# Performance work log

Hardware: AMD Instinct MI355X
Metric: run time of the kernel (lower is better)

## Reference

```python
import jax, jax.numpy as jnp
import numpy as np

B, T, C = 4, 2048, 1024
N_HEADS = 16
HEAD_DIM = C // N_HEADS


def setup_inputs() -> dict:
    key = jax.random.key(0)
    k1, k2, k3 = jax.random.split(key, 3)
    x = jax.random.normal(k1, (B, T, C), dtype=jnp.float32)
    w_qkv = jax.random.normal(k2, (C, 3 * C), dtype=jnp.float32) * (1.0 / np.sqrt(C))
    w_proj = jax.random.normal(k3, (C, C), dtype=jnp.float32) * (1.0 / np.sqrt(C))
    return {"x": x, "w_qkv": w_qkv, "w_proj": w_proj}


def reference(x, w_qkv, w_proj):
    b, t, c = x.shape
    qkv = x @ w_qkv                                  # [B,T,3C]
    q, k, v = jnp.split(qkv, 3, axis=-1)
    def split_heads(u):
        return u.reshape(b, t, N_HEADS, HEAD_DIM).transpose(0, 2, 1, 3)  # [B,H,T,D]
    q, k, v = split_heads(q), split_heads(k), split_heads(v)
    scale = 1.0 / np.sqrt(HEAD_DIM)
    att = jnp.einsum('bhqd,bhkd->bhqk', q, k) * scale   # [B,H,T,T]
    causal = jnp.tril(jnp.ones((t, t), dtype=bool))
    att = jnp.where(causal[None, None], att, -jnp.inf)
    att = jax.nn.softmax(att, axis=-1)
    out = jnp.einsum('bhqk,bhkd->bhqd', att, v)         # [B,H,T,D]
    out = out.transpose(0, 2, 1, 3).reshape(b, t, c)
    return out @ w_proj
```

## Files before the change

### kernel.cpp

```cpp
#include <hip/hip_runtime.h>
#include <hip/hip_bf16.h>
#include <stdint.h>

typedef __bf16 bf16_t;
typedef __bf16 bf16x4 __attribute__((ext_vector_type(4)));
typedef __bf16 bf16x8 __attribute__((ext_vector_type(8)));
typedef float  f32x4  __attribute__((ext_vector_type(4)));

#define B_    4
#define T_    2048
#define C_    1024
#define NH    16
#define HD    64
#define M_TOT (B_ * T_)

__device__ __forceinline__ void gload16(const void* g, void* l) {
    __builtin_amdgcn_global_load_lds(
        (const __attribute__((address_space(1))) uint32_t*)g,
        (__attribute__((address_space(3))) uint32_t*)l, 16, 0, 0);
}

__global__ void conv_x_kernel(const float* __restrict__ x, bf16_t* __restrict__ xb, int n4) {
    int i = blockIdx.x * blockDim.x + threadIdx.x;
    int stride = gridDim.x * blockDim.x;
    for (; i < n4; i += stride) {
        float4 v = reinterpret_cast<const float4*>(x)[i];
        union { bf16_t h[4]; uint2 u; } p;
        p.h[0] = (bf16_t)v.x; p.h[1] = (bf16_t)v.y;
        p.h[2] = (bf16_t)v.z; p.h[3] = (bf16_t)v.w;
        reinterpret_cast<uint2*>(xb)[i] = p.u;
    }
}

__global__ void transpose_w_kernel(const float* __restrict__ w, bf16_t* __restrict__ wt,
                                   int K, int N) {
    __shared__ float tile[32][33];
    int n0 = blockIdx.x * 32, k0 = blockIdx.y * 32;
    int tx = threadIdx.x, ty = threadIdx.y;
    #pragma unroll
    for (int i = 0; i < 32; i += 8)
        tile[ty + i][tx] = w[(size_t)(k0 + ty + i) * N + n0 + tx];
    __syncthreads();
    #pragma unroll
    for (int i = 0; i < 32; i += 8)
        wt[(size_t)(n0 + ty + i) * K + k0 + tx] = (bf16_t)tile[tx][ty + i];
}

#define QSCALE 0.18033688011112042f

#define LA0 0
#define LA1 16384
#define LB0 32768
#define LB1 49152

#define GST(ptr, rbase, base, kt) do { int k0_ = ((kt) << 6) & (K - 1);           \
    _Pragma("unroll") for (int c_ = 0; c_ < 4; ++c_) {                            \
        int li_ = tid + c_ * 256; int row_ = li_ >> 3;                            \
        int sw_ = (li_ & 7) ^ (row_ & 7);                                         \
        gload16(ptr + (size_t)((rbase) + row_) * K + k0_ + sw_ * 8,               \
                lds + (base) + li_ * 16); } } while (0)

#define GREAD(abase, bbase) do {                                                  \
    _Pragma("unroll") for (int mi_ = 0; mi_ < 4; ++mi_)                           \
        _Pragma("unroll") for (int kk_ = 0; kk_ < 2; ++kk_) {                     \
            int row_  = wm * 64 + mi_ * 16 + q16;                                 \
            int byte_ = (row_ * 128 + kk_ * 64 + g * 16) ^ ((row_ & 7) << 4);     \
            af[mi_ * 2 + kk_] = *reinterpret_cast<const bf16x8*>(lds + (abase) + byte_); } \
    _Pragma("unroll") for (int n_ = 0; n_ < 4; ++n_)                              \
        _Pragma("unroll") for (int kk_ = 0; kk_ < 2; ++kk_) {                     \
            int row_  = wn * 64 + n_ * 16 + q16;                                  \
            int byte_ = (row_ * 128 + kk_ * 64 + g * 16) ^ ((row_ & 7) << 4);     \
            bfr[n_ * 2 + kk_] = *reinterpret_cast<const bf16x8*>(lds + (bbase) + byte_); } } while (0)

#define GMFMA(milo) do { __builtin_amdgcn_s_setprio(1);                           \
    _Pragma("unroll") for (int mi_ = 0; mi_ < 2; ++mi_)                           \
        _Pragma("unroll") for (int kk_ = 0; kk_ < 2; ++kk_)                       \
            _Pragma("unroll") for (int n_ = 0; n_ < 4; ++n_)                      \
                acc[(milo) + mi_][n_] = __builtin_amdgcn_mfma_f32_16x16x32_bf16(  \
                    af[((milo) + mi_) * 2 + kk_], bfr[n_ * 2 + kk_],              \
                    acc[(milo) + mi_][n_], 0, 0, 0);                              \
    __builtin_amdgcn_s_setprio(0); } while (0)

template<int MODE>
__global__ __launch_bounds__(256, 2) void gemm_kernel(
    const bf16_t* __restrict__ A, const bf16_t* __restrict__ Bt,
    float* __restrict__ Cout,
    bf16_t* __restrict__ Qo, bf16_t* __restrict__ Ko, bf16_t* __restrict__ Vt,
    int M, int N, int K)
{
    __shared__ __align__(16) char lds[65536];
    const int tid  = threadIdx.x;
    const int lane = tid & 63;
    const int wid  = tid >> 6;
    const int wm   = wid >> 1, wn = wid & 1;
    const int q16  = lane & 15, g = lane >> 4;
    const int xcd = blockIdx.x & 7;
    const int i0  = blockIdx.x >> 3;
    const int mbase = (xcd * 8 + (i0 & 7)) * 128;
    const int nbase = (i0 >> 3) * 128;
    const int NITER = K >> 7;

    f32x4  acc[4][4] = {};
    bf16x8 af[8], bfr[8];

    GST(A, mbase, LA0, 0); GST(Bt, nbase, LB0, 0);
    GST(A, mbase, LA1, 1); GST(Bt, nbase, LB1, 1);
    asm volatile("s_waitcnt vmcnt(8)" ::: "memory");
    __builtin_amdgcn_s_barrier();
    __builtin_amdgcn_sched_barrier(0);

    #pragma unroll 1
    for (int i = 0; i < NITER; ++i) {
        GREAD(LA0, LB0);
        __builtin_amdgcn_s_barrier();
        asm volatile("s_waitcnt lgkmcnt(0)" ::: "memory");
        __builtin_amdgcn_sched_barrier(0);
        GMFMA(0);
        __builtin_amdgcn_s_barrier();
        GST(A, mbase, LA0, 2 * i + 2); GST(Bt, nbase, LB0, 2 * i + 2);
        __builtin_amdgcn_sched_barrier(0);
        GMFMA(2);
        asm volatile("s_waitcnt vmcnt(8)" ::: "memory");
        __builtin_amdgcn_s_barrier();
        GREAD(LA1, LB1);
        __builtin_amdgcn_s_barrier();
        asm volatile("s_waitcnt lgkmcnt(0)" ::: "memory");
        __builtin_amdgcn_sched_barrier(0);
        GMFMA(0);
        __builtin_amdgcn_s_barrier();
        GST(A, mbase, LA1, 2 * i + 3); GST(Bt, nbase, LB1, 2 * i + 3);
        __builtin_amdgcn_sched_barrier(0);
        GMFMA(2);
        asm volatile("s_waitcnt vmcnt(8)" ::: "memory");
        __builtin_amdgcn_s_barrier();
    }
    asm volatile("s_waitcnt vmcnt(0)" ::: "memory");

    #pragma unroll
    for (int mi = 0; mi < 4; ++mi) {
        #pragma unroll
        for (int n = 0; n < 4; ++n) {
            const int row0 = mbase + wm * 64 + mi * 16 + g * 4;
            const int col0 = nbase + wn * 64 + n * 16;
            if (MODE == 0) {
                #pragma unroll
                for (int r = 0; r < 4; ++r)
                    Cout[(size_t)(row0 + r) * N + col0 + q16] = acc[mi][n][r];
            } else {
                const int b = row0 >> 11, t0 = row0 & 2047;
                if (col0 < 1024) {
                    int h = col0 >> 6, d = (col0 & 63) + q16;
                    #pragma unroll
                    for (int r = 0; r < 4; ++r)
                        Qo[((size_t)(b * NH + h) * T_ + t0 + r) * HD + d] =
                            (bf16_t)(acc[mi][n][r] * QSCALE);
                } else if (col0 < 2048) {
                    int h = (col0 - 1024) >> 6, d = (col0 & 63) + q16;
                    #pragma unroll
                    for (int r = 0; r < 4; ++r)
                        Ko[((size_t)(b * NH + h) * T_ + t0 + r) * HD + d] =
                            (bf16_t)acc[mi][n][r];
                } else {
                    int h = (col0 - 2048) >> 6, d = (col0 & 63) + q16;
                    bf16x4 vv = { (bf16_t)acc[mi][n][0], (bf16_t)acc[mi][n][1],
                                  (bf16_t)acc[mi][n][2], (bf16_t)acc[mi][n][3] };
                    *reinterpret_cast<bf16x4*>(
                        Vt + ((size_t)(b * NH + h) * HD + d) * T_ + t0) = vv;
                }
            }
        }
    }
}

__global__ __launch_bounds__(256, 3) void attn_kernel(
    const bf16_t* __restrict__ Q, const bf16_t* __restrict__ K,
    const bf16_t* __restrict__ Vt, bf16_t* __restrict__ out)
{
    __shared__ __align__(16) char kvbuf[2][16384];
    __shared__ __align__(16) char plds[4][4096];
    const int tid  = threadIdx.x;
    const int lane = tid & 63;
    const int wid  = tid >> 6;
    const int g    = lane >> 4;
    const int q16  = lane & 15;

    const int bid = blockIdx.x;
    const int k   = bid >> 6;
    const int bh  = bid & 63;
    const int b   = bh >> 4, h = bh & 15;
    const int qt  = (k < 4) ? (15 - k) : (k < 8) ? (k + 4) : (k < 12) ? (k - 4) : (15 - k);

    const bf16_t* Qh = Q  + (size_t)bh * T_ * HD;
    const bf16_t* Kh = K  + (size_t)bh * T_ * HD;
    const bf16_t* Vh = Vt + (size_t)bh * HD * T_;
    char* myp = plds[wid];
    const int pswz = (q16 & 7) << 4;

    const int nt    = 2 * qt + 2;
    const int qbase = qt * 128 + wid * 32;
    const int qg0   = qbase + q16;
    const int qg1   = qbase + 16 + q16;

    int koff[4][2], pwoff[4], proff[2];
    #pragma unroll
    for (int t = 0; t < 4; ++t) {
        #pragma unroll
        for (int kk = 0; kk < 2; ++kk)
            koff[t][kk] = ((t * 16 + q16) * 128 + kk * 64 + g * 16) ^ pswz;
        pwoff[t] = (q16 * 128 + t * 32 + g * 8) ^ pswz;
    }
    proff[0] = (q16 * 128 + g * 16) ^ pswz;
    proff[1] = (q16 * 128 + 64 + g * 16) ^ pswz;

    const int li0 = tid,        row0 = li0 >> 3, sw0 = (li0 & 7) ^ (row0 & 7);
    const int li1 = tid + 256,  row1 = li1 >> 3, sw1 = (li1 & 7) ^ (row1 & 7);
    const bf16_t* kS0 = Kh + (size_t)row0 * HD + sw0 * 8;
    const bf16_t* kS1 = Kh + (size_t)row1 * HD + sw1 * 8;
    const bf16_t* vS0 = Vh + (size_t)row0 * T_ + sw0 * 8;
    const bf16_t* vS1 = Vh + (size_t)row1 * T_ + sw1 * 8;

#define STAGE2(buf) do {                                                          \
        gload16(kS0, (char*)(buf) + tid * 16);                                    \
        gload16(kS1, (char*)(buf) + 4096 + tid * 16);                             \
        gload16(vS0, (char*)(buf) + 8192 + tid * 16);                             \
        gload16(vS1, (char*)(buf) + 12288 + tid * 16);                            \
        kS0 += 4096; kS1 += 4096; vS0 += 64; vS1 += 64; } while (0)

    bf16x8 qf0[2], qf1[2];
    #pragma unroll
    for (int kk = 0; kk < 2; ++kk) {
        qf0[kk] = *reinterpret_cast<const bf16x8*>(Qh + (size_t)qg0 * HD + kk * 32 + g * 8);
        qf1[kk] = *reinterpret_cast<const bf16x8*>(Qh + (size_t)qg1 * HD + kk * 32 + g * 8);
    }

    f32x4 acc0[4] = {}, acc1[4] = {};
    float l0 = 0.f, l1 = 0.f;

#define ABODY(IT, CURB, NXTB) do {                                                \
    const int kv0 = (IT) << 6;                                                    \
    if ((IT) + 1 < nt) {                                                          \
        STAGE2(NXTB);                                                             \
        asm volatile("s_waitcnt vmcnt(4)" ::: "memory");                          \
    } else {                                                                      \
        asm volatile("s_waitcnt vmcnt(0)" ::: "memory");                          \
    }                                                                             \
    __builtin_amdgcn_s_barrier();                                                 \
    __builtin_amdgcn_sched_barrier(0);                                            \
    const char* Kl = (const char*)(CURB);                                         \
    const char* Vl = (const char*)(CURB) + 8192;                                  \
    f32x4 s0[4] = {}, s1[4] = {};                                                 \
    __builtin_amdgcn_s_setprio(1);                                                \
    _Pragma("unroll") for (int t = 0; t < 4; ++t)                                 \
        _Pragma("unroll") for (int kk = 0; kk < 2; ++kk) {                        \
            bf16x8 kf = *reinterpret_cast<const bf16x8*>(Kl + koff[t][kk]);       \
            s0[t] = __builtin_amdgcn_mfma_f32_16x16x32_bf16(kf, qf0[kk], s0[t], 0, 0, 0); \
            s1[t] = __builtin_amdgcn_mfma_f32_16x16x32_bf16(kf, qf1[kk], s1[t], 0, 0, 0); } \
    __builtin_amdgcn_s_setprio(0);                                                \
    if (kv0 + 63 > qbase) {                                                       \
        _Pragma("unroll") for (int t = 0; t < 4; ++t)                             \
            _Pragma("unroll") for (int r = 0; r < 4; ++r) {                       \
                int kv = kv0 + t * 16 + g * 4 + r;                                \
                if (kv > qg0) s0[t][r] = -1e30f;                                  \
                if (kv > qg1) s1[t][r] = -1e30f; } }                              \
    _Pragma("unroll") for (int t = 0; t < 4; ++t) {                               \
        float p00 = exp2f(s0[t][0]), p01 = exp2f(s0[t][1]);                       \
        float p02 = exp2f(s0[t][2]), p03 = exp2f(s0[t][3]);                       \
        l0 += (p00 + p01) + (p02 + p03);                                          \
        bf16x4 pw0 = { (bf16_t)p00, (bf16_t)p01, (bf16_t)p02, (bf16_t)p03 };      \
        *reinterpret_cast<bf16x4*>(myp + pwoff[t]) = pw0;                         \
        float p10 = exp2f(s1[t][0]), p11 = exp2f(s1[t][1]);                       \
        float p12 = exp2f(s1[t][2]), p13 = exp2f(s1[t][3]);                       \
        l1 += (p10 + p11) + (p12 + p13);                                          \
        bf16x4 pw1 = { (bf16_t)p10, (bf16_t)p11, (bf16_t)p12, (bf16_t)p13 };      \
        *reinterpret_cast<bf16x4*>(myp + 2048 + pwoff[t]) = pw1; }                \
    asm volatile("s_waitcnt lgkmcnt(0)" ::: "memory");                            \
    __builtin_amdgcn_sched_barrier(0);                                            \
    bf16x8 pf0[2], pf1[2];                                                        \
    _Pragma("unroll") for (int kk2 = 0; kk2 < 2; ++kk2) {                         \
        pf0[kk2] = *reinterpret_cast<const bf16x8*>(myp + proff[kk2]);            \
        pf1[kk2] = *reinterpret_cast<const bf16x8*>(myp + 2048 + proff[kk2]); }   \
    __builtin_amdgcn_s_setprio(1);                                                \
    _Pragma("unroll") for (int nf = 0; nf < 4; ++nf)                              \
        _Pragma("unroll") for (int kk2 = 0; kk2 < 2; ++kk2) {                     \
            bf16x8 vf = *reinterpret_cast<const bf16x8*>(Vl + koff[nf][kk2]);     \
            acc0[nf] = __builtin_amdgcn_mfma_f32_16x16x32_bf16(vf, pf0[kk2], acc0[nf], 0, 0, 0); \
            acc1[nf] = __builtin_amdgcn_mfma_f32_16x16x32_bf16(vf, pf1[kk2], acc1[nf], 0, 0, 0); } \
    __builtin_amdgcn_s_setprio(0);                                                \
    asm volatile("s_waitcnt lgkmcnt(0)" ::: "memory");                            \
    __builtin_amdgcn_s_barrier();                                                 \
} while (0)

    STAGE2(kvbuf[0]);
    #pragma unroll 1
    for (int it = 0; it < nt; it += 2) {
        ABODY(it,     kvbuf[0], kvbuf[1]);
        ABODY(it + 1, kvbuf[1], kvbuf[0]);
    }

    l0 += __shfl_xor(l0, 16, 64);
    l0 += __shfl_xor(l0, 32, 64);
    l1 += __shfl_xor(l1, 16, 64);
    l1 += __shfl_xor(l1, 32, 64);
    float inv0 = 1.f / l0, inv1 = 1.f / l1;
    #pragma unroll
    for (int nf = 0; nf < 4; ++nf) {
        bf16x4 ov0 = { (bf16_t)(acc0[nf][0] * inv0), (bf16_t)(acc0[nf][1] * inv0),
                       (bf16_t)(acc0[nf][2] * inv0), (bf16_t)(acc0[nf][3] * inv0) };
        *reinterpret_cast<bf16x4*>(
            out + (size_t)(b * T_ + qg0) * C_ + h * HD + nf * 16 + g * 4) = ov0;
        bf16x4 ov1 = { (bf16_t)(acc1[nf][0] * inv1), (bf16_t)(acc1[nf][1] * inv1),
                       (bf16_t)(acc1[nf][2] * inv1), (bf16_t)(acc1[nf][3] * inv1) };
        *reinterpret_cast<bf16x4*>(
            out + (size_t)(b * T_ + qg1) * C_ + h * HD + nf * 16 + g * 4) = ov1;
    }
#undef ABODY
#undef STAGE2
}

extern "C" void kernel_launch(void* const* d_in, const int* in_sizes, int n_in,
                              void* d_out, int out_size, void* d_ws, size_t ws_size,
                              hipStream_t stream) {
    const float* x      = (const float*)d_in[0];
    const float* w_qkv  = (const float*)d_in[1];
    const float* w_proj = (const float*)d_in[2];
    float* out = (float*)d_out;

    char* ws = (char*)d_ws;
    bf16_t* xb     = (bf16_t*)(ws);
    bf16_t* wqkvT  = (bf16_t*)(ws + 16777216);
    bf16_t* wprojT = (bf16_t*)(ws + 23068672);
    bf16_t* Qb     = (bf16_t*)(ws + 25165824);
    bf16_t* Kb     = (bf16_t*)(ws + 41943040);
    bf16_t* Vtb    = (bf16_t*)(ws + 58720256);
    bf16_t* attnb  = (bf16_t*)(ws + 75497472);

    conv_x_kernel<<<2048, 256, 0, stream>>>(x, xb, (B_ * T_ * C_) / 4);
    transpose_w_kernel<<<dim3(3 * C_ / 32, C_ / 32), dim3(32, 8), 0, stream>>>(w_qkv, wqkvT, C_, 3 * C_);
    transpose_w_kernel<<<dim3(C_ / 32, C_ / 32), dim3(32, 8), 0, stream>>>(w_proj, wprojT, C_, C_);

    gemm_kernel<1><<<1536, 256, 0, stream>>>(
        xb, wqkvT, nullptr, Qb, Kb, Vtb, M_TOT, 3 * C_, C_);

    attn_kernel<<<1024, 256, 0, stream>>>(Qb, Kb, Vtb, attnb);

    gemm_kernel<0><<<512, 256, 0, stream>>>(
        attnb, wprojT, out, nullptr, nullptr, nullptr, M_TOT, C_, C_);
}
```

Measured before the change: 160.1 us.

## Load V fragments directly from global into registers, stage only K in LDS

The attention kernel stops staging V tiles through LDS. Each wave now loads its own V fragments straight from global memory into registers at the start of every iteration, and the vmcnt waits are adjusted so the PV MFMAs wait only for those loads. This halves the LDS footprint per block, and launch bounds are raised to 4 blocks per SM for more occupancy. The cost is that each wave issues redundant uncoalesced global reads of V (every wave reads the same 64x64 tile), which raises L2 traffic and register pressure.

```diff
diff --git a/kernel.cpp b/kernel.cpp
--- a/kernel.cpp
+++ b/kernel.cpp
@@ -172,11 +172,11 @@
     }
 }
 
-__global__ __launch_bounds__(256, 3) void attn_kernel(
+__global__ __launch_bounds__(256, 4) void attn_kernel(
     const bf16_t* __restrict__ Q, const bf16_t* __restrict__ K,
     const bf16_t* __restrict__ Vt, bf16_t* __restrict__ out)
 {
-    __shared__ __align__(16) char kvbuf[2][16384];
+    __shared__ __align__(16) char kbuf[2][8192];
     __shared__ __align__(16) char plds[4][4096];
     const int tid  = threadIdx.x;
     const int lane = tid & 63;
@@ -216,15 +216,16 @@
     const int li1 = tid + 256,  row1 = li1 >> 3, sw1 = (li1 & 7) ^ (row1 & 7);
     const bf16_t* kS0 = Kh + (size_t)row0 * HD + sw0 * 8;
     const bf16_t* kS1 = Kh + (size_t)row1 * HD + sw1 * 8;
-    const bf16_t* vS0 = Vh + (size_t)row0 * T_ + sw0 * 8;
-    const bf16_t* vS1 = Vh + (size_t)row1 * T_ + sw1 * 8;
-
-#define STAGE2(buf) do {                                                          \
+
+    const bf16_t* vP0 = Vh + (size_t)(0 * 16 + q16) * T_ + g * 8;
+    const bf16_t* vP1 = Vh + (size_t)(1 * 16 + q16) * T_ + g * 8;
+    const bf16_t* vP2 = Vh + (size_t)(2 * 16 + q16) * T_ + g * 8;
+    const bf16_t* vP3 = Vh + (size_t)(3 * 16 + q16) * T_ + g * 8;
+
+#define STAGEK(buf) do {                                                          \
         gload16(kS0, (char*)(buf) + tid * 16);                                    \
         gload16(kS1, (char*)(buf) + 4096 + tid * 16);                             \
-        gload16(vS0, (char*)(buf) + 8192 + tid * 16);                             \
-        gload16(vS1, (char*)(buf) + 12288 + tid * 16);                            \
-        kS0 += 4096; kS1 += 4096; vS0 += 64; vS1 += 64; } while (0)
+        kS0 += 4096; kS1 += 4096; } while (0)
 
     bf16x8 qf0[2], qf1[2];
     #pragma unroll
@@ -238,16 +239,26 @@
 
 #define ABODY(IT, CURB, NXTB) do {                                                \
     const int kv0 = (IT) << 6;                                                    \
+                      \
+    bf16x8 vf[8];                                                                 \
+    vf[0] = *reinterpret_cast<const bf16x8*>(vP0);                                \
+    vf[1] = *reinterpret_cast<const bf16x8*>(vP0 + 32);                           \
+    vf[2] = *reinterpret_cast<const bf16x8*>(vP1);                                \
+    vf[3] = *reinterpret_cast<const bf16x8*>(vP1 + 32);                           \
+    vf[4] = *reinterpret_cast<const bf16x8*>(vP2);                                \
+    vf[5] = *reinterpret_cast<const bf16x8*>(vP2 + 32);                           \
+    vf[6] = *reinterpret_cast<const bf16x8*>(vP3);                                \
+    vf[7] = *reinterpret_cast<const bf16x8*>(vP3 + 32);                           \
+    vP0 += 64; vP1 += 64; vP2 += 64; vP3 += 64;                                   \
     if ((IT) + 1 < nt) {                                                          \
-        STAGE2(NXTB);                                                             \
-        asm volatile("s_waitcnt vmcnt(4)" ::: "memory");                          \
+        STAGEK(NXTB);                                                             \
+        asm volatile("s_waitcnt vmcnt(10)" ::: "memory");        \
     } else {                                                                      \
-        asm volatile("s_waitcnt vmcnt(0)" ::: "memory");                          \
+        asm volatile("s_waitcnt vmcnt(8)" ::: "memory");                          \
     }                                                                             \
     __builtin_amdgcn_s_barrier();                                                 \
     __builtin_amdgcn_sched_barrier(0);                                            \
     const char* Kl = (const char*)(CURB);                                         \
-    const char* Vl = (const char*)(CURB) + 8192;                                  \
     f32x4 s0[4] = {}, s1[4] = {};                                                 \
     __builtin_amdgcn_s_setprio(1);                                                \
     _Pragma("unroll") for (int t = 0; t < 4; ++t)                                 \
@@ -279,22 +290,28 @@
     _Pragma("unroll") for (int kk2 = 0; kk2 < 2; ++kk2) {                         \
         pf0[kk2] = *reinterpret_cast<const bf16x8*>(myp + proff[kk2]);            \
         pf1[kk2] = *reinterpret_cast<const bf16x8*>(myp + 2048 + proff[kk2]); }   \
+    if ((IT) + 1 < nt) {                                                          \
+        asm volatile("s_waitcnt vmcnt(2)" ::: "memory");         \
+    } else {                                                                      \
+        asm volatile("s_waitcnt vmcnt(0)" ::: "memory");                          \
+    }                                                                             \
     __builtin_amdgcn_s_setprio(1);                                                \
     _Pragma("unroll") for (int nf = 0; nf < 4; ++nf)                              \
         _Pragma("unroll") for (int kk2 = 0; kk2 < 2; ++kk2) {                     \
-            bf16x8 vf = *reinterpret_cast<const bf16x8*>(Vl + koff[nf][kk2]);     \
-            acc0[nf] = __builtin_amdgcn_mfma_f32_16x16x32_bf16(vf, pf0[kk2], acc0[nf], 0, 0, 0); \
-            acc1[nf] = __builtin_amdgcn_mfma_f32_16x16x32_bf16(vf, pf1[kk2], acc1[nf], 0, 0, 0); } \
+            acc0[nf] = __builtin_amdgcn_mfma_f32_16x16x32_bf16(                   \
+                vf[nf * 2 + kk2], pf0[kk2], acc0[nf], 0, 0, 0);                   \
+            acc1[nf] = __builtin_amdgcn_mfma_f32_16x16x32_bf16(                   \
+                vf[nf * 2 + kk2], pf1[kk2], acc1[nf], 0, 0, 0); }                 \
     __builtin_amdgcn_s_setprio(0);                                                \
     asm volatile("s_waitcnt lgkmcnt(0)" ::: "memory");                            \
     __builtin_amdgcn_s_barrier();                                                 \
 } while (0)
 
-    STAGE2(kvbuf[0]);
+    STAGEK(kbuf[0]);
     #pragma unroll 1
     for (int it = 0; it < nt; it += 2) {
-        ABODY(it,     kvbuf[0], kvbuf[1]);
-        ABODY(it + 1, kvbuf[1], kvbuf[0]);
+        ABODY(it,     kbuf[0], kbuf[1]);
+        ABODY(it + 1, kbuf[1], kbuf[0]);
     }
 
     l0 += __shfl_xor(l0, 16, 64);
@@ -314,7 +331,7 @@
             out + (size_t)(b * T_ + qg1) * C_ + h * HD + nf * 16 + g * 4) = ov1;
     }
 #undef ABODY
-#undef STAGE2
+#undef STAGEK
 }
 
 extern "C" void kernel_launch(void* const* d_in, const int* in_sizes, int n_in,
```

Measured after the change: 415.4 us. +159.4%, slower.
